# Performance work log

Hardware: AMD Instinct MI355X
Metric: run time of the kernel (lower is better)

The kernel has to match this reference:

```python
import jax, jax.numpy as jnp
import numpy as np

N_NODES = 50000
N_EDGES = 800000
STALK_DIM = 16
N_TYPES = 16


def setup_inputs() -> dict:
    key = jax.random.key(0)
    k1, k2, k3, k4 = jax.random.split(key, 4)
    entity_reps = jax.random.normal(k1, (STALK_DIM, N_NODES), dtype=jnp.float32)
    restriction_maps = jax.random.normal(k2, (N_TYPES, N_TYPES, STALK_DIM, STALK_DIM), dtype=jnp.float32)
    edge_index = jax.random.randint(k3, (2, N_EDGES), 0, N_NODES, dtype=jnp.int64 if jax.config.jax_enable_x64 else jnp.int32).astype(jnp.int32)
    entity_types = jax.random.randint(k4, (N_NODES,), 0, N_TYPES).astype(jnp.int32)
    return {"entity_reps": entity_reps, "restriction_maps": restriction_maps,
            "edge_index": edge_index, "entity_types": entity_types}


def reference(entity_reps, restriction_maps, edge_index, entity_types):
    src, dst = edge_index[0], edge_index[1]
    n_nodes = entity_reps.shape[1]

    # deg^{-1/2} from in-degree on dst (col), inf -> 0 for isolated nodes
    deg = jax.ops.segment_sum(jnp.ones_like(src, dtype=entity_reps.dtype), dst,
                              num_segments=n_nodes)
    inv_deg = jnp.where(deg > 0, jax.lax.rsqrt(jnp.maximum(deg, 1.0)), 0.0)

    # normalized reps: x @ diag(inv_deg)  -> scale each node column
    x = entity_reps * inv_deg[None, :]            # [d, n_nodes]

    t_src = entity_types[src]                     # [E]
    t_dst = entity_types[dst]
    head_maps = restriction_maps[t_src, t_dst]    # [E, d, d]
    tail_maps = restriction_maps[t_dst, t_src]    # [E, d, d]

    x_src = x[:, src].T                           # [E, d]
    x_dst = x[:, dst].T                           # [E, d]
    head_emb = jnp.einsum('eij,ej->ei', head_maps, x_src)  # [E, d]
    tail_emb = jnp.einsum('eij,ej->ei', tail_maps, x_dst)  # [E, d]

    # scatter-add head at src, subtract tail at dst
    comparison = (jax.ops.segment_sum(head_emb, src, num_segments=n_nodes)
                  - jax.ops.segment_sum(tail_emb, dst, num_segments=n_nodes))  # [n_nodes, d]

    # sum over d of ||comparison[:, j]||^2 == total sum of squares
    return jnp.sum(comparison * comparison)
```

## Files before the change

kernel.cpp:

```cpp
#include <hip/hip_runtime.h>

constexpr int NNODES_C = 50000;
constexpr int D = 16;
constexpr int NT = 16;
constexpr int E_C = 800000;

constexpr int NODE_P = 128;
constexpr int NPART  = 391;
constexpr int CHUNK  = 4096;
constexpr int NBLK   = 196;
constexpr int SLOT   = 64;
constexpr int BLK_E  = NPART * SLOT;

constexpr size_t OFF_ENT   = 0;
constexpr size_t OFF_CNT   = (size_t)NBLK * BLK_E * 2;
constexpr size_t FAST_NEED = OFF_CNT + (size_t)NBLK * NPART * 4;

constexpr size_t F_TCNT  = 3200000;
constexpr size_t F_TLIST = 3200064;



__global__ __launch_bounds__(512)
void scatter_kernel(const int* __restrict__ ei, const int* __restrict__ types,
                    unsigned short* __restrict__ entries,
                    unsigned int* __restrict__ cnt_g,
                    float* __restrict__ out, int E) {
    __shared__ unsigned short stage[BLK_E];
    __shared__ unsigned int   cur[NPART];
    const int tid = threadIdx.x;
    const int b   = blockIdx.x;
    if (b == 0 && tid == 0) out[0] = 0.0f;
    if (tid < NPART) cur[tid] = 0;
    __syncthreads();

    const int start = b * CHUNK;
    const int end   = min(start + CHUNK, E);
    const int e0    = start + tid * 8;

    if (e0 + 7 < end) {
        const int4 sa = *reinterpret_cast<const int4*>(ei + e0);
        const int4 sb = *reinterpret_cast<const int4*>(ei + e0 + 4);
        const int4 da = *reinterpret_cast<const int4*>(ei + E + e0);
        const int4 db = *reinterpret_cast<const int4*>(ei + E + e0 + 4);
        const unsigned int ss[8] = {(unsigned int)sa.x, (unsigned int)sa.y,
                                    (unsigned int)sa.z, (unsigned int)sa.w,
                                    (unsigned int)sb.x, (unsigned int)sb.y,
                                    (unsigned int)sb.z, (unsigned int)sb.w};
        const unsigned int dd[8] = {(unsigned int)da.x, (unsigned int)da.y,
                                    (unsigned int)da.z, (unsigned int)da.w,
                                    (unsigned int)db.x, (unsigned int)db.y,
                                    (unsigned int)db.z, (unsigned int)db.w};
        unsigned int ts[8], td[8];
        #pragma unroll
        for (int k = 0; k < 8; ++k) { ts[k] = (unsigned int)types[ss[k]];
                                      td[k] = (unsigned int)types[dd[k]]; }
        #pragma unroll
        for (int k = 0; k < 8; ++k) {
            const unsigned int ps = atomicAdd(&cur[ss[k] >> 7], 1u);
            stage[(ss[k] >> 7) * SLOT + ps] =
                (unsigned short)(((ss[k] & 127u) << 5) | td[k]);
            const unsigned int pd = atomicAdd(&cur[dd[k] >> 7], 1u);
            stage[(dd[k] >> 7) * SLOT + pd] =
                (unsigned short)(((dd[k] & 127u) << 5) | 0x10u | ts[k]);
        }
    } else if (e0 < end) {
        for (int e = e0; e < end; ++e) {
            const unsigned int s = (unsigned int)ei[e];
            const unsigned int d = (unsigned int)ei[E + e];
            const unsigned int ps = atomicAdd(&cur[s >> 7], 1u);
            stage[(s >> 7) * SLOT + ps] =
                (unsigned short)(((s & 127u) << 5) | (unsigned int)types[d]);
            const unsigned int pd = atomicAdd(&cur[d >> 7], 1u);
            stage[(d >> 7) * SLOT + pd] =
                (unsigned short)(((d & 127u) << 5) | 0x10u | (unsigned int)types[s]);
        }
    }
    __syncthreads();

    {
        const uint4* sg  = reinterpret_cast<const uint4*>(stage);
        uint4*       dst = reinterpret_cast<uint4*>(entries + (size_t)b * BLK_E);
        for (int i = tid; i < BLK_E / 8; i += 512) dst[i] = sg[i];
        unsigned int* cdst = cnt_g + (size_t)b * NPART;
        if (tid < NPART) cdst[tid] = cur[tid];
    }
}

__global__ __launch_bounds__(512)
void hist_node_kernel(const float* __restrict__ reps,
                      const float* __restrict__ rmaps,
                      const unsigned short* __restrict__ entries,
                      const unsigned int* __restrict__ cnt_g,
                      const int* __restrict__ types,
                      float* __restrict__ out, int N) {
    __shared__ unsigned int  hist[NODE_P * 17];
    __shared__ float         C[NODE_P][16];
    __shared__ float         X[NODE_P][16];
    __shared__ unsigned char llist[NT * NODE_P];
    __shared__ float         IDG[NODE_P];
    __shared__ int           lcnt[NT];
    __shared__ unsigned int  cnt_s[NBLK];
    __shared__ float         wpart[8];

    const int tid = threadIdx.x;
    const int p   = blockIdx.x;
    const int n0  = p * NODE_P;
    const int nn  = min(NODE_P, N - n0);

    {
        const int rg = tid >> 7;
        const int tt = tid & 127;
        if (tt < nn) {
            #pragma unroll
            for (int j = 0; j < 4; ++j)
                X[tt][rg * 4 + j] = reps[(rg * 4 + j) * N + n0 + tt];
        }
    }
    for (int i = tid; i < NODE_P * 17; i += 512) hist[i] = 0u;
    if (tid < NT) lcnt[tid] = 0;
    if (tid < NBLK) cnt_s[tid] = cnt_g[(size_t)tid * NPART + p];
    __syncthreads();

    if (tid < 2 * NBLK) {
        const int sb = tid >> 1;
        const unsigned int cnt = cnt_s[sb];
        const uint4* src = reinterpret_cast<const uint4*>(
            entries + (size_t)sb * BLK_E + p * SLOT);
        const int nch = (int)((cnt + 7) >> 3);
        for (int c = (tid & 1); c < nch; c += 2) {
            const uint4 v = src[c];
            const unsigned int words[4] = {v.x, v.y, v.z, v.w};
            const unsigned int base = (unsigned int)c * 8;
            #pragma unroll
            for (int k = 0; k < 4; ++k) {
                #pragma unroll
                for (int h = 0; h < 2; ++h) {
                    const unsigned int idx = base + k * 2 + h;
                    if (idx < cnt) {
                        const unsigned int e = (words[k] >> (h * 16)) & 0xFFFFu;
                        atomicAdd(&hist[(e >> 5) * 17 + (e & 15u)],
                                  1u << (e & 0x10u));
                    }
                }
            }
        }
    }
    __syncthreads();

    if (tid < nn) {
        unsigned int deg = 0;
        #pragma unroll
        for (int t = 0; t < NT; ++t) deg += (hist[tid * 17 + t] >> 16);
        #pragma unroll
        for (int t = 0; t < NT; ++t) {
            const unsigned int hw = hist[tid * 17 + t];
            C[tid][t] = (float)((int)(hw & 0xFFFFu) - (int)(hw >> 16));
        }
        IDG[tid] = (deg > 0) ? (1.0f / (float)deg) : 0.0f;
        const int ty = types[n0 + tid];
        const int rk = atomicAdd(&lcnt[ty], 1);
        llist[ty * NODE_P + rk] = (unsigned char)tid;
    }
    __syncthreads();

    const int wv = tid >> 6;
    const int l  = tid & 63;
    const int tg = l >> 4;
    const int r  = l & 15;

    float part = 0.0f;
    for (int ty = wv * 2; ty < wv * 2 + 2; ++ty) {
        const int m = lcnt[ty];
        if (m == 0) continue;

        float4 Rf[4][4];
        const float* Rbase = rmaps + (((size_t)ty * NT + tg * 4) * D + r) * D;
        #pragma unroll
        for (int jt = 0; jt < 4; ++jt)
            #pragma unroll
            for (int q = 0; q < 4; ++q)
                Rf[jt][q] = *reinterpret_cast<const float4*>(Rbase + jt * D * D + q * 4);

        for (int idx = 0; idx < m; ++idx) {
            const int nl = llist[ty * NODE_P + idx];
            const float4 x0 = *reinterpret_cast<const float4*>(&X[nl][0]);
            const float4 x1 = *reinterpret_cast<const float4*>(&X[nl][4]);
            const float4 x2 = *reinterpret_cast<const float4*>(&X[nl][8]);
            const float4 x3 = *reinterpret_cast<const float4*>(&X[nl][12]);
            const float4 c4 = *reinterpret_cast<const float4*>(&C[nl][tg * 4]);
            const float idg = IDG[nl];
            const float ca[4] = {c4.x, c4.y, c4.z, c4.w};

            float y = 0.0f;
            #pragma unroll
            for (int jt = 0; jt < 4; ++jt) {
                float s = 0.0f;
                s = fmaf(Rf[jt][0].x, x0.x, s); s = fmaf(Rf[jt][0].y, x0.y, s);
                s = fmaf(Rf[jt][0].z, x0.z, s); s = fmaf(Rf[jt][0].w, x0.w, s);
                s = fmaf(Rf[jt][1].x, x1.x, s); s = fmaf(Rf[jt][1].y, x1.y, s);
                s = fmaf(Rf[jt][1].z, x1.z, s); s = fmaf(Rf[jt][1].w, x1.w, s);
                s = fmaf(Rf[jt][2].x, x2.x, s); s = fmaf(Rf[jt][2].y, x2.y, s);
                s = fmaf(Rf[jt][2].z, x2.z, s); s = fmaf(Rf[jt][2].w, x2.w, s);
                s = fmaf(Rf[jt][3].x, x3.x, s); s = fmaf(Rf[jt][3].y, x3.y, s);
                s = fmaf(Rf[jt][3].z, x3.z, s); s = fmaf(Rf[jt][3].w, x3.w, s);
                y = fmaf(ca[jt], s, y);
            }
            y += __shfl_xor(y, 16);
            y += __shfl_xor(y, 32);
            if (l < 16) part = fmaf(y * y, idg, part);
        }
    }

    #pragma unroll
    for (int off = 32; off > 0; off >>= 1)
        part += __shfl_down(part, off);
    if (l == 0) wpart[wv] = part;
    __syncthreads();
    if (tid == 0) {
        float v = 0.0f;
        #pragma unroll
        for (int i = 0; i < 8; ++i) v += wpart[i];
        if (v != 0.0f) atomicAdd(out, v);
    }
}


__global__ __launch_bounds__(256)
void edge_kernel(const int* __restrict__ ei, const int* __restrict__ types,
                 unsigned int* __restrict__ pk, int E) {
    const int i = (blockIdx.x * blockDim.x + threadIdx.x) * 4;
    if (i >= E) return;
    if (i + 3 < E) {
        const int4 s4 = *reinterpret_cast<const int4*>(ei + i);
        const int4 t4 = *reinterpret_cast<const int4*>(ei + E + i);
        const int ss[4] = {s4.x, s4.y, s4.z, s4.w};
        const int tt[4] = {t4.x, t4.y, t4.z, t4.w};
        #pragma unroll
        for (int k = 0; k < 4; ++k) {
            atomicAdd(&pk[ss[k] * NT + types[tt[k]]], 1u);
            atomicAdd(&pk[tt[k] * NT + types[ss[k]]], 0x10000u);
        }
    } else {
        for (int e = i; e < E; ++e) {
            const int s = ei[e];
            const int t = ei[E + e];
            atomicAdd(&pk[s * NT + types[t]], 1u);
            atomicAdd(&pk[t * NT + types[s]], 0x10000u);
        }
    }
}

__global__ __launch_bounds__(256)
void list_kernel(const int* __restrict__ types,
                 int* __restrict__ tcnt, int* __restrict__ tlist, int N) {
    __shared__ int lcnt[NT];
    __shared__ int lbase[NT];
    if (threadIdx.x < NT) lcnt[threadIdx.x] = 0;
    __syncthreads();
    const int n = blockIdx.x * 256 + threadIdx.x;
    int ty = 0, lr = 0;
    const bool valid = (n < N);
    if (valid) {
        ty = types[n];
        lr = atomicAdd(&lcnt[ty], 1);
    }
    __syncthreads();
    if (threadIdx.x < NT)
        lbase[threadIdx.x] = atomicAdd(&tcnt[threadIdx.x], lcnt[threadIdx.x]);
    __syncthreads();
    if (valid)
        tlist[ty * NNODES_C + lbase[ty] + lr] = n;
}

__global__ __launch_bounds__(256)
void node_kernel(const float* __restrict__ reps,
                 const float* __restrict__ rmaps,
                 const unsigned int* __restrict__ pk,
                 const int* __restrict__ tcnt,
                 const int* __restrict__ tlist,
                 float* __restrict__ out, int N) {
    const int ty  = blockIdx.y;
    const int cnt = tcnt[ty];
    if ((int)(blockIdx.x * 64) >= cnt) return;

    const int tid = threadIdx.x;
    const int w   = tid >> 6;
    const int l   = tid & 63;
    const int tg  = l >> 4;
    const int r   = l & 15;

    float4 Rf[4][4];
    {
        const float* Rbase = rmaps + (((size_t)ty * NT + tg * 4) * D + r) * D;
        #pragma unroll
        for (int jt = 0; jt < 4; ++jt)
            #pragma unroll
            for (int q = 0; q < 4; ++q)
                Rf[jt][q] = *reinterpret_cast<const float4*>(Rbase + jt * D * D + q * 4);
    }

    __shared__ int   NI[64];
    __shared__ float X[64][16];
    __shared__ float C[64][16];
    __shared__ int   PD[64][4];
    __shared__ float IDG[64];

    float part = 0.0f;

    for (int base = blockIdx.x * 64; base < cnt; base += gridDim.x * 64) {
        const int nb = min(64, cnt - base);

        __syncthreads();
        if (tid < nb) NI[tid] = tlist[ty * NNODES_C + base + tid];
        __syncthreads();

        const int b = tid >> 2, q = tid & 3;
        if (b < nb) {
            const int n = NI[b];
            const uint4 pw = reinterpret_cast<const uint4*>(pk + (size_t)n * NT)[q];
            const unsigned int ws4[4] = {pw.x, pw.y, pw.z, pw.w};
            int hsum = 0;
            #pragma unroll
            for (int j = 0; j < 4; ++j) {
                const int hi = (int)(ws4[j] >> 16);
                const int lo = (int)(ws4[j] & 0xFFFFu);
                C[b][q * 4 + j] = (float)(lo - hi);
                hsum += hi;
            }
            PD[b][q] = hsum;
            #pragma unroll
            for (int j = 0; j < 4; ++j)
                X[b][q * 4 + j] = reps[(q * 4 + j) * N + n];
        }
        __syncthreads();
        if (tid < nb) {
            const int dg = PD[tid][0] + PD[tid][1] + PD[tid][2] + PD[tid][3];
            IDG[tid] = (dg > 0) ? (1.0f / (float)dg) : 0.0f;
        }
        __syncthreads();

        for (int bb = w; bb < nb; bb += 4) {
            const float4 x0 = *reinterpret_cast<const float4*>(&X[bb][0]);
            const float4 x1 = *reinterpret_cast<const float4*>(&X[bb][4]);
            const float4 x2 = *reinterpret_cast<const float4*>(&X[bb][8]);
            const float4 x3 = *reinterpret_cast<const float4*>(&X[bb][12]);
            const float4 c4 = *reinterpret_cast<const float4*>(&C[bb][tg * 4]);
            const float idg = IDG[bb];
            const float ca[4] = {c4.x, c4.y, c4.z, c4.w};

            float y = 0.0f;
            #pragma unroll
            for (int jt = 0; jt < 4; ++jt) {
                float s = 0.0f;
                s = fmaf(Rf[jt][0].x, x0.x, s); s = fmaf(Rf[jt][0].y, x0.y, s);
                s = fmaf(Rf[jt][0].z, x0.z, s); s = fmaf(Rf[jt][0].w, x0.w, s);
                s = fmaf(Rf[jt][1].x, x1.x, s); s = fmaf(Rf[jt][1].y, x1.y, s);
                s = fmaf(Rf[jt][1].z, x1.z, s); s = fmaf(Rf[jt][1].w, x1.w, s);
                s = fmaf(Rf[jt][2].x, x2.x, s); s = fmaf(Rf[jt][2].y, x2.y, s);
                s = fmaf(Rf[jt][2].z, x2.z, s); s = fmaf(Rf[jt][2].w, x2.w, s);
                s = fmaf(Rf[jt][3].x, x3.x, s); s = fmaf(Rf[jt][3].y, x3.y, s);
                s = fmaf(Rf[jt][3].z, x3.z, s); s = fmaf(Rf[jt][3].w, x3.w, s);
                y = fmaf(ca[jt], s, y);
            }
            y += __shfl_xor(y, 16);
            y += __shfl_xor(y, 32);
            if (l < 16) part = fmaf(y * y, idg, part);
        }
    }

    #pragma unroll
    for (int off = 32; off > 0; off >>= 1)
        part += __shfl_down(part, off);
    __shared__ float wpart[4];
    if (l == 0) wpart[w] = part;
    __syncthreads();
    if (tid == 0) {
        const float v = wpart[0] + wpart[1] + wpart[2] + wpart[3];
        if (v != 0.0f) atomicAdd(out, v);
    }
}

extern "C" void kernel_launch(void* const* d_in, const int* in_sizes, int n_in,
                              void* d_out, int out_size, void* d_ws, size_t ws_size,
                              hipStream_t stream) {
    const float* reps  = (const float*)d_in[0];
    const float* rmaps = (const float*)d_in[1];
    const int*   ei    = (const int*)d_in[2];
    const int*   types = (const int*)d_in[3];
    float* out = (float*)d_out;

    const int E = in_sizes[2] / 2;
    const int N = in_sizes[3];

    char* ws = (char*)d_ws;
    const bool fast = (N == NNODES_C && E == E_C && ws_size >= FAST_NEED);

    if (fast) {
        unsigned short* entries = (unsigned short*)(ws + OFF_ENT);
        unsigned int*   cnt_g   = (unsigned int*)(ws + OFF_CNT);

        scatter_kernel  <<<NBLK,  512, 0, stream>>>(ei, types, entries, cnt_g, out, E);
        hist_node_kernel<<<NPART, 512, 0, stream>>>(reps, rmaps, entries, cnt_g,
                                                    types, out, N);
    } else {
        unsigned int* pk = (unsigned int*)ws;
        int* tcnt  = (int*)(ws + F_TCNT);
        int* tlist = (int*)(ws + F_TLIST);

        hipMemsetAsync(d_ws, 0, F_TLIST, stream);
        hipMemsetAsync(d_out, 0, sizeof(float), stream);
        edge_kernel<<<(E / 4 + 255) / 256, 256, 0, stream>>>(ei, types, pk, E);
        list_kernel<<<(N + 255) / 256, 256, 0, stream>>>(types, tcnt, tlist, N);
        dim3 grid(52, NT);
        node_kernel<<<grid, 256, 0, stream>>>(reps, rmaps, pk, tcnt, tlist, out, N);
    }
}
```

Before: 36.18 us.

## Compact per-block staging buckets with prefix-scan offsets instead of fixed slots

```diff
diff --git a/kernel.cpp b/kernel.cpp
--- a/kernel.cpp
+++ b/kernel.cpp
@@ -9,12 +9,12 @@
 constexpr int NPART  = 391;
 constexpr int CHUNK  = 4096;
 constexpr int NBLK   = 196;
-constexpr int SLOT   = 64;
-constexpr int BLK_E  = NPART * SLOT;
+constexpr int BLK_E  = 2 * CHUNK;
 
 constexpr size_t OFF_ENT   = 0;
 constexpr size_t OFF_CNT   = (size_t)NBLK * BLK_E * 2;
-constexpr size_t FAST_NEED = OFF_CNT + (size_t)NBLK * NPART * 4;
+constexpr size_t OFF_OFF   = OFF_CNT + (size_t)NBLK * NPART * 4;
+constexpr size_t FAST_NEED = OFF_OFF + (size_t)NBLK * NPART * 4;
 
 constexpr size_t F_TCNT  = 3200000;
 constexpr size_t F_TLIST = 3200064;
@@ -25,65 +25,82 @@
 void scatter_kernel(const int* __restrict__ ei, const int* __restrict__ types,
                     unsigned short* __restrict__ entries,
                     unsigned int* __restrict__ cnt_g,
+                    unsigned int* __restrict__ off_g,
                     float* __restrict__ out, int E) {
     __shared__ unsigned short stage[BLK_E];
-    __shared__ unsigned int   cur[NPART];
+    __shared__ unsigned int   cnt[NPART];
+    __shared__ unsigned int   off[NPART];
+    __shared__ unsigned int   scanbuf[512];
     const int tid = threadIdx.x;
     const int b   = blockIdx.x;
     if (b == 0 && tid == 0) out[0] = 0.0f;
-    if (tid < NPART) cur[tid] = 0;
+    if (tid < NPART) cnt[tid] = 0;
     __syncthreads();
 
     const int start = b * CHUNK;
     const int end   = min(start + CHUNK, E);
     const int e0    = start + tid * 8;
-
+    unsigned int ss[8], dd[8], ts[8], td[8];
+    int ne = 0;
     if (e0 + 7 < end) {
         const int4 sa = *reinterpret_cast<const int4*>(ei + e0);
-        const int4 sb = *reinterpret_cast<const int4*>(ei + e0 + 4);
+        const int4 sb4 = *reinterpret_cast<const int4*>(ei + e0 + 4);
         const int4 da = *reinterpret_cast<const int4*>(ei + E + e0);
         const int4 db = *reinterpret_cast<const int4*>(ei + E + e0 + 4);
-        const unsigned int ss[8] = {(unsigned int)sa.x, (unsigned int)sa.y,
-                                    (unsigned int)sa.z, (unsigned int)sa.w,
-                                    (unsigned int)sb.x, (unsigned int)sb.y,
-                                    (unsigned int)sb.z, (unsigned int)sb.w};
-        const unsigned int dd[8] = {(unsigned int)da.x, (unsigned int)da.y,
-                                    (unsigned int)da.z, (unsigned int)da.w,
-                                    (unsigned int)db.x, (unsigned int)db.y,
-                                    (unsigned int)db.z, (unsigned int)db.w};
-        unsigned int ts[8], td[8];
-        #pragma unroll
-        for (int k = 0; k < 8; ++k) { ts[k] = (unsigned int)types[ss[k]];
-                                      td[k] = (unsigned int)types[dd[k]]; }
-        #pragma unroll
-        for (int k = 0; k < 8; ++k) {
-            const unsigned int ps = atomicAdd(&cur[ss[k] >> 7], 1u);
-            stage[(ss[k] >> 7) * SLOT + ps] =
-                (unsigned short)(((ss[k] & 127u) << 5) | td[k]);
-            const unsigned int pd = atomicAdd(&cur[dd[k] >> 7], 1u);
-            stage[(dd[k] >> 7) * SLOT + pd] =
-                (unsigned short)(((dd[k] & 127u) << 5) | 0x10u | ts[k]);
-        }
-    } else if (e0 < end) {
+        ss[0]=(unsigned)sa.x; ss[1]=(unsigned)sa.y; ss[2]=(unsigned)sa.z; ss[3]=(unsigned)sa.w;
+        ss[4]=(unsigned)sb4.x; ss[5]=(unsigned)sb4.y; ss[6]=(unsigned)sb4.z; ss[7]=(unsigned)sb4.w;
+        dd[0]=(unsigned)da.x; dd[1]=(unsigned)da.y; dd[2]=(unsigned)da.z; dd[3]=(unsigned)da.w;
+        dd[4]=(unsigned)db.x; dd[5]=(unsigned)db.y; dd[6]=(unsigned)db.z; dd[7]=(unsigned)db.w;
+        ne = 8;
+    } else {
         for (int e = e0; e < end; ++e) {
-            const unsigned int s = (unsigned int)ei[e];
-            const unsigned int d = (unsigned int)ei[E + e];
-            const unsigned int ps = atomicAdd(&cur[s >> 7], 1u);
-            stage[(s >> 7) * SLOT + ps] =
-                (unsigned short)(((s & 127u) << 5) | (unsigned int)types[d]);
-            const unsigned int pd = atomicAdd(&cur[d >> 7], 1u);
-            stage[(d >> 7) * SLOT + pd] =
-                (unsigned short)(((d & 127u) << 5) | 0x10u | (unsigned int)types[s]);
-        }
+            ss[ne] = (unsigned int)ei[e];
+            dd[ne] = (unsigned int)ei[E + e];
+            ++ne;
+        }
+    }
+    for (int k = 0; k < ne; ++k) { ts[k] = (unsigned int)types[ss[k]];
+                                   td[k] = (unsigned int)types[dd[k]]; }
+
+    for (int k = 0; k < ne; ++k) {
+        atomicAdd(&cnt[ss[k] >> 7], 1u);
+        atomicAdd(&cnt[dd[k] >> 7], 1u);
+    }
+    __syncthreads();
+
+    unsigned int v = (tid < NPART) ? cnt[tid] : 0u;
+    scanbuf[tid] = v;
+    __syncthreads();
+    #pragma unroll
+    for (int dstep = 1; dstep < 512; dstep <<= 1) {
+        const unsigned int add = (tid >= dstep) ? scanbuf[tid - dstep] : 0u;
+        __syncthreads();
+        scanbuf[tid] += add;
+        __syncthreads();
+    }
+    if (tid < NPART) off[tid] = scanbuf[tid] - cnt[tid];
+    __syncthreads();
+    if (tid < NPART) scanbuf[tid] = off[tid];
+    __syncthreads();
+    unsigned int* cur = scanbuf;
+
+    for (int k = 0; k < ne; ++k) {
+        const unsigned int ps = atomicAdd(&cur[ss[k] >> 7], 1u);
+        stage[ps] = (unsigned short)(((ss[k] & 127u) << 5) | td[k]);
+        const unsigned int pd = atomicAdd(&cur[dd[k] >> 7], 1u);
+        stage[pd] = (unsigned short)(((dd[k] & 127u) << 5) | 0x10u | ts[k]);
     }
     __syncthreads();
 
     {
         const uint4* sg  = reinterpret_cast<const uint4*>(stage);
         uint4*       dst = reinterpret_cast<uint4*>(entries + (size_t)b * BLK_E);
+        #pragma unroll
         for (int i = tid; i < BLK_E / 8; i += 512) dst[i] = sg[i];
-        unsigned int* cdst = cnt_g + (size_t)b * NPART;
-        if (tid < NPART) cdst[tid] = cur[tid];
+        if (tid < NPART) {
+            cnt_g[(size_t)b * NPART + tid] = cnt[tid];
+            off_g[(size_t)b * NPART + tid] = off[tid];
+        }
     }
 }
 
@@ -92,6 +109,7 @@
                       const float* __restrict__ rmaps,
                       const unsigned short* __restrict__ entries,
                       const unsigned int* __restrict__ cnt_g,
+                      const unsigned int* __restrict__ off_g,
                       const int* __restrict__ types,
                       float* __restrict__ out, int N) {
     __shared__ unsigned int  hist[NODE_P * 17];
@@ -101,6 +119,7 @@
     __shared__ float         IDG[NODE_P];
     __shared__ int           lcnt[NT];
     __shared__ unsigned int  cnt_s[NBLK];
+    __shared__ unsigned int  off_s[NBLK];
     __shared__ float         wpart[8];
 
     const int tid = threadIdx.x;
@@ -120,30 +139,19 @@
     for (int i = tid; i < NODE_P * 17; i += 512) hist[i] = 0u;
     if (tid < NT) lcnt[tid] = 0;
     if (tid < NBLK) cnt_s[tid] = cnt_g[(size_t)tid * NPART + p];
+    else if (tid >= 256 && tid < 256 + NBLK)
+        off_s[tid - 256] = off_g[(size_t)(tid - 256) * NPART + p];
     __syncthreads();
 
     if (tid < 2 * NBLK) {
         const int sb = tid >> 1;
         const unsigned int cnt = cnt_s[sb];
-        const uint4* src = reinterpret_cast<const uint4*>(
-            entries + (size_t)sb * BLK_E + p * SLOT);
-        const int nch = (int)((cnt + 7) >> 3);
-        for (int c = (tid & 1); c < nch; c += 2) {
-            const uint4 v = src[c];
-            const unsigned int words[4] = {v.x, v.y, v.z, v.w};
-            const unsigned int base = (unsigned int)c * 8;
-            #pragma unroll
-            for (int k = 0; k < 4; ++k) {
-                #pragma unroll
-                for (int h = 0; h < 2; ++h) {
-                    const unsigned int idx = base + k * 2 + h;
-                    if (idx < cnt) {
-                        const unsigned int e = (words[k] >> (h * 16)) & 0xFFFFu;
-                        atomicAdd(&hist[(e >> 5) * 17 + (e & 15u)],
-                                  1u << (e & 0x10u));
-                    }
-                }
-            }
+        const unsigned int off = off_s[sb];
+        const unsigned short* src = entries + (size_t)sb * BLK_E + off;
+        for (unsigned int i = (tid & 1); i < cnt; i += 2) {
+            const unsigned int e = src[i];
+            atomicAdd(&hist[(e >> 5) * 17 + (e & 15u)],
+                      1u << (e & 0x10u));
         }
     }
     __syncthreads();
@@ -399,10 +407,12 @@
     if (fast) {
         unsigned short* entries = (unsigned short*)(ws + OFF_ENT);
         unsigned int*   cnt_g   = (unsigned int*)(ws + OFF_CNT);
-
-        scatter_kernel  <<<NBLK,  512, 0, stream>>>(ei, types, entries, cnt_g, out, E);
+        unsigned int*   off_g   = (unsigned int*)(ws + OFF_OFF);
+
+        scatter_kernel  <<<NBLK,  512, 0, stream>>>(ei, types, entries, cnt_g,
+                                                    off_g, out, E);
         hist_node_kernel<<<NPART, 512, 0, stream>>>(reps, rmaps, entries, cnt_g,
-                                                    types, out, N);
+                                                    off_g, types, out, N);
     } else {
         unsigned int* pk = (unsigned int*)ws;
         int* tcnt  = (int*)(ws + F_TCNT);
```

Measured after the change: 41.99 us. 16.1% more time.

## Split each node partition across two half-size blocks in hist_node_kernel

Applied to the files above, without the earlier changes.

```diff
diff --git a/kernel.cpp b/kernel.cpp
--- a/kernel.cpp
+++ b/kernel.cpp
@@ -11,6 +11,9 @@
 constexpr int NBLK   = 196;
 constexpr int SLOT   = 64;
 constexpr int BLK_E  = NPART * SLOT;
+
+constexpr int NODE_H  = 64;
+constexpr int NPART_H = 782;
 
 constexpr size_t OFF_ENT   = 0;
 constexpr size_t OFF_CNT   = (size_t)NBLK * BLK_E * 2;
@@ -87,48 +90,49 @@
     }
 }
 
-__global__ __launch_bounds__(512)
+__global__ __launch_bounds__(256)
 void hist_node_kernel(const float* __restrict__ reps,
                       const float* __restrict__ rmaps,
                       const unsigned short* __restrict__ entries,
                       const unsigned int* __restrict__ cnt_g,
                       const int* __restrict__ types,
                       float* __restrict__ out, int N) {
-    __shared__ unsigned int  hist[NODE_P * 17];
-    __shared__ float         C[NODE_P][16];
-    __shared__ float         X[NODE_P][16];
-    __shared__ unsigned char llist[NT * NODE_P];
-    __shared__ float         IDG[NODE_P];
+    __shared__ unsigned int  hist[NODE_H * 17];
+    __shared__ float         C[NODE_H][16];
+    __shared__ float         X[NODE_H][16];
+    __shared__ unsigned char llist[NT * NODE_H];
+    __shared__ float         IDG[NODE_H];
     __shared__ int           lcnt[NT];
     __shared__ unsigned int  cnt_s[NBLK];
-    __shared__ float         wpart[8];
-
-    const int tid = threadIdx.x;
-    const int p   = blockIdx.x;
-    const int n0  = p * NODE_P;
-    const int nn  = min(NODE_P, N - n0);
+    __shared__ float         wpart[4];
+
+    const int tid  = threadIdx.x;
+    const int p    = blockIdx.x;
+    const int ppar = p >> 1;
+    const unsigned int sub = (unsigned int)(p & 1);
+    const int n0   = p * NODE_H;
+    const int nn   = min(NODE_H, N - n0);
 
     {
-        const int rg = tid >> 7;
-        const int tt = tid & 127;
+        const int rg = tid >> 6;
+        const int tt = tid & 63;
         if (tt < nn) {
             #pragma unroll
             for (int j = 0; j < 4; ++j)
                 X[tt][rg * 4 + j] = reps[(rg * 4 + j) * N + n0 + tt];
         }
     }
-    for (int i = tid; i < NODE_P * 17; i += 512) hist[i] = 0u;
+    for (int i = tid; i < NODE_H * 17; i += 256) hist[i] = 0u;
     if (tid < NT) lcnt[tid] = 0;
-    if (tid < NBLK) cnt_s[tid] = cnt_g[(size_t)tid * NPART + p];
-    __syncthreads();
-
-    if (tid < 2 * NBLK) {
-        const int sb = tid >> 1;
-        const unsigned int cnt = cnt_s[sb];
+    if (tid < NBLK) cnt_s[tid] = cnt_g[(size_t)tid * NPART + ppar];
+    __syncthreads();
+
+    if (tid < NBLK) {
+        const unsigned int cnt = cnt_s[tid];
         const uint4* src = reinterpret_cast<const uint4*>(
-            entries + (size_t)sb * BLK_E + p * SLOT);
+            entries + (size_t)tid * BLK_E + ppar * SLOT);
         const int nch = (int)((cnt + 7) >> 3);
-        for (int c = (tid & 1); c < nch; c += 2) {
+        for (int c = 0; c < nch; ++c) {
             const uint4 v = src[c];
             const unsigned int words[4] = {v.x, v.y, v.z, v.w};
             const unsigned int base = (unsigned int)c * 8;
@@ -139,8 +143,9 @@
                     const unsigned int idx = base + k * 2 + h;
                     if (idx < cnt) {
                         const unsigned int e = (words[k] >> (h * 16)) & 0xFFFFu;
-                        atomicAdd(&hist[(e >> 5) * 17 + (e & 15u)],
-                                  1u << (e & 0x10u));
+                        if (((e >> 11) & 1u) == sub)
+                            atomicAdd(&hist[((e >> 5) & 63u) * 17 + (e & 15u)],
+                                      1u << (e & 0x10u));
                     }
                 }
             }
@@ -160,7 +165,7 @@
         IDG[tid] = (deg > 0) ? (1.0f / (float)deg) : 0.0f;
         const int ty = types[n0 + tid];
         const int rk = atomicAdd(&lcnt[ty], 1);
-        llist[ty * NODE_P + rk] = (unsigned char)tid;
+        llist[ty * NODE_H + rk] = (unsigned char)tid;
     }
     __syncthreads();
 
@@ -170,7 +175,7 @@
     const int r  = l & 15;
 
     float part = 0.0f;
-    for (int ty = wv * 2; ty < wv * 2 + 2; ++ty) {
+    for (int ty = wv * 4; ty < wv * 4 + 4; ++ty) {
         const int m = lcnt[ty];
         if (m == 0) continue;
 
@@ -183,7 +188,7 @@
                 Rf[jt][q] = *reinterpret_cast<const float4*>(Rbase + jt * D * D + q * 4);
 
         for (int idx = 0; idx < m; ++idx) {
-            const int nl = llist[ty * NODE_P + idx];
+            const int nl = llist[ty * NODE_H + idx];
             const float4 x0 = *reinterpret_cast<const float4*>(&X[nl][0]);
             const float4 x1 = *reinterpret_cast<const float4*>(&X[nl][4]);
             const float4 x2 = *reinterpret_cast<const float4*>(&X[nl][8]);
@@ -218,9 +223,7 @@
     if (l == 0) wpart[wv] = part;
     __syncthreads();
     if (tid == 0) {
-        float v = 0.0f;
-        #pragma unroll
-        for (int i = 0; i < 8; ++i) v += wpart[i];
+        const float v = wpart[0] + wpart[1] + wpart[2] + wpart[3];
         if (v != 0.0f) atomicAdd(out, v);
     }
 }
@@ -400,9 +403,9 @@
         unsigned short* entries = (unsigned short*)(ws + OFF_ENT);
         unsigned int*   cnt_g   = (unsigned int*)(ws + OFF_CNT);
 
-        scatter_kernel  <<<NBLK,  512, 0, stream>>>(ei, types, entries, cnt_g, out, E);
-        hist_node_kernel<<<NPART, 512, 0, stream>>>(reps, rmaps, entries, cnt_g,
-                                                    types, out, N);
+        scatter_kernel  <<<NBLK,    512, 0, stream>>>(ei, types, entries, cnt_g, out, E);
+        hist_node_kernel<<<NPART_H, 256, 0, stream>>>(reps, rmaps, entries, cnt_g,
+                                                      types, out, N);
     } else {
         unsigned int* pk = (unsigned int*)ws;
         int* tcnt  = (int*)(ws + F_TCNT);
```

After: 48.28 us. 33.5% more time.

## Transpose staged edge entries to partition-major layout for contiguous reads

Applied to the files above, without the earlier changes.

```diff
diff --git a/kernel.cpp b/kernel.cpp
--- a/kernel.cpp
+++ b/kernel.cpp
@@ -10,11 +10,11 @@
 constexpr int CHUNK  = 4096;
 constexpr int NBLK   = 196;
 constexpr int SLOT   = 64;
-constexpr int BLK_E  = NPART * SLOT;
+constexpr int P_PITCH = NBLK * SLOT;
 
 constexpr size_t OFF_ENT   = 0;
-constexpr size_t OFF_CNT   = (size_t)NBLK * BLK_E * 2;
-constexpr size_t FAST_NEED = OFF_CNT + (size_t)NBLK * NPART * 4;
+constexpr size_t OFF_CNT   = (size_t)NPART * P_PITCH * 2;
+constexpr size_t FAST_NEED = OFF_CNT + (size_t)NPART * NBLK * 4;
 
 constexpr size_t F_TCNT  = 3200000;
 constexpr size_t F_TLIST = 3200064;
@@ -26,7 +26,7 @@
                     unsigned short* __restrict__ entries,
                     unsigned int* __restrict__ cnt_g,
                     float* __restrict__ out, int E) {
-    __shared__ unsigned short stage[BLK_E];
+    __shared__ unsigned short stage[NPART * SLOT];
     __shared__ unsigned int   cur[NPART];
     const int tid = threadIdx.x;
     const int b   = blockIdx.x;
@@ -80,10 +80,12 @@
 
     {
         const uint4* sg  = reinterpret_cast<const uint4*>(stage);
-        uint4*       dst = reinterpret_cast<uint4*>(entries + (size_t)b * BLK_E);
-        for (int i = tid; i < BLK_E / 8; i += 512) dst[i] = sg[i];
-        unsigned int* cdst = cnt_g + (size_t)b * NPART;
-        if (tid < NPART) cdst[tid] = cur[tid];
+        uint4*       dst = reinterpret_cast<uint4*>(entries);
+        for (int i = tid; i < NPART * 8; i += 512) {
+            const int s = i >> 3, j = i & 7;
+            dst[(size_t)s * (P_PITCH / 8) + b * 8 + j] = sg[i];
+        }
+        if (tid < NPART) cnt_g[(size_t)tid * NBLK + b] = cur[tid];
     }
 }
 
@@ -119,25 +121,25 @@
     }
     for (int i = tid; i < NODE_P * 17; i += 512) hist[i] = 0u;
     if (tid < NT) lcnt[tid] = 0;
-    if (tid < NBLK) cnt_s[tid] = cnt_g[(size_t)tid * NPART + p];
-    __syncthreads();
-
-    if (tid < 2 * NBLK) {
-        const int sb = tid >> 1;
-        const unsigned int cnt = cnt_s[sb];
+    if (tid < NBLK) cnt_s[tid] = cnt_g[(size_t)p * NBLK + tid];
+    __syncthreads();
+
+    {
         const uint4* src = reinterpret_cast<const uint4*>(
-            entries + (size_t)sb * BLK_E + p * SLOT);
-        const int nch = (int)((cnt + 7) >> 3);
-        for (int c = (tid & 1); c < nch; c += 2) {
-            const uint4 v = src[c];
+            entries + (size_t)p * P_PITCH);
+        for (int g = tid; g < NBLK * 8; g += 512) {
+            const unsigned int cnt   = cnt_s[g >> 3];
+            const unsigned int cbase = (unsigned int)(g & 7) * 8;
+            if (cbase >= cnt) continue;
+            const uint4 v = src[g];
             const unsigned int words[4] = {v.x, v.y, v.z, v.w};
-            const unsigned int base = (unsigned int)c * 8;
+            const unsigned int rem = cnt - cbase;
             #pragma unroll
             for (int k = 0; k < 4; ++k) {
                 #pragma unroll
                 for (int h = 0; h < 2; ++h) {
-                    const unsigned int idx = base + k * 2 + h;
-                    if (idx < cnt) {
+                    const unsigned int idx = (unsigned int)(k * 2 + h);
+                    if (idx < rem) {
                         const unsigned int e = (words[k] >> (h * 16)) & 0xFFFFu;
                         atomicAdd(&hist[(e >> 5) * 17 + (e & 15u)],
                                   1u << (e & 0x10u));
```

Measured after the change: 37.20 us. +2.8%, slower.
